# Kernel tuning notes

Hardware: AMD Instinct MI355X
Metric: run time of the kernel (lower is better)

The kernel has to match this reference:

```python
import jax, jax.numpy as jnp
import numpy as np

H, D = 16, 1024
HD = D // H  # 64

def setup_inputs() -> dict:
    key = jax.random.key(0)
    ks = jax.random.split(key, 11)
    B, S = 2, 2048
    s_in = 1.0 / np.sqrt(D)
    return {
        "V": jax.random.normal(ks[0], (B, S, D), jnp.float32),
        "K": jax.random.normal(ks[1], (B, S, D), jnp.float32),
        "Q": jax.random.normal(ks[2], (B, S, D), jnp.float32),
        # stacked per-head Linear weights, torch layout [out,in] -> [H, HD, D]
        "Wv": jax.random.normal(ks[3], (H, HD, D), jnp.float32) * s_in,
        "bv": jnp.zeros((H, HD), jnp.float32),
        "Wk": jax.random.normal(ks[4], (H, HD, D), jnp.float32) * s_in,
        "bk": jnp.zeros((H, HD), jnp.float32),
        "Wq": jax.random.normal(ks[5], (H, HD, D), jnp.float32) * s_in,
        "bq": jnp.zeros((H, HD), jnp.float32),
        "Wo": jax.random.normal(ks[6], (D, D), jnp.float32) * s_in,
        "bo": jnp.zeros((D,), jnp.float32),
    }

def reference(V, K, Q, Wv, bv, Wk, bk, Wq, bq, Wo, bo):
    scale = HD ** (-0.5)
    # per-head projections fused into one batched GEMM: [B,S,D] x [H,HD,D] -> [B,H,S,HD]
    q = jnp.einsum('bsd,hed->bhse', Q, Wq) + bq[None, :, None, :]
    k = jnp.einsum('bsd,hed->bhse', K, Wk) + bk[None, :, None, :]
    v = jnp.einsum('bsd,hed->bhse', V, Wv) + bv[None, :, None, :]
    # scaled dot-product attention
    scores = jnp.einsum('bhqe,bhke->bhqk', q, k) * scale  # [B,H,S,S]
    p = jax.nn.softmax(scores, axis=-1)
    att = jnp.einsum('bhqk,bhke->bhqe', p, v)  # [B,H,S,HD]
    # concat heads (head 0 first, matching the torch cat order) then output proj
    B, _, S, _ = att.shape
    cat = jnp.transpose(att, (0, 2, 1, 3)).reshape(B, S, H * HD)
    return cat @ Wo.T + bo
```

## Files before the change

### kernel.cpp

```cpp
#include <hip/hip_runtime.h>
#include <cstdint>
#include <cstddef>

typedef __bf16 bf16_t;
typedef bf16_t bf16x8 __attribute__((ext_vector_type(8)));
typedef bf16_t bf16x4 __attribute__((ext_vector_type(4)));
typedef float f32x4 __attribute__((ext_vector_type(4)));
typedef float f32x2 __attribute__((ext_vector_type(2)));

__device__ __forceinline__ void gl_lds16(const void* g, void* l) {
  __builtin_amdgcn_global_load_lds(
      (const __attribute__((address_space(1))) void*)g,
      (__attribute__((address_space(3))) void*)l, 16, 0, 0);
}

__device__ __forceinline__ f32x4 mfma16(bf16x8 a, bf16x8 b, f32x4 c) {
  return __builtin_amdgcn_mfma_f32_16x16x32_bf16(a, b, c, 0, 0, 0);
}

__device__ __forceinline__ float exp2_fast(float x) {
  float r;
  asm("v_exp_f32 %0, %1" : "=v"(r) : "v"(x));
  return r;
}

#define SCHED_FENCE() __builtin_amdgcn_sched_barrier(0)
#define WAIT_VM0()   do { asm volatile("s_waitcnt vmcnt(0)");   SCHED_FENCE(); } while (0)
#define WAIT_LGKM0() do { asm volatile("s_waitcnt lgkmcnt(0)"); SCHED_FENCE(); } while (0)
#define RAW_BAR()    do { __builtin_amdgcn_s_barrier();         SCHED_FENCE(); } while (0)

struct CvtArgs { const float* src[7]; bf16_t* dst[7]; };

__global__ __launch_bounds__(256) void convert_all(CvtArgs a) {
  unsigned g = blockIdx.x * 256u + threadIdx.x;
  unsigned seg, off;
  if (g < 524288u) {
    seg = g >> 17; off = g & 131071u;
  } else {
    unsigned h = g - 524288u;
    seg = 4u + (h >> 19); off = h & 524287u;
  }
  const float4* s = (const float4*)a.src[seg] + (size_t)off * 2;
  float4 x0 = s[0], x1 = s[1];
  bf16x8 o;
  o[0] = (bf16_t)x0.x; o[1] = (bf16_t)x0.y; o[2] = (bf16_t)x0.z; o[3] = (bf16_t)x0.w;
  o[4] = (bf16_t)x1.x; o[5] = (bf16_t)x1.y; o[6] = (bf16_t)x1.z; o[7] = (bf16_t)x1.w;
  *(bf16x8*)(a.dst[seg] + (size_t)off * 8) = o;
}

__device__ __forceinline__ void stage128(const bf16_t* src, bf16_t* dst, int t, int w) {
  #pragma unroll
  for (int i = 0; i < 4; i++) {
    int g = t + i * 256;
    int r = g >> 3, pc = g & 7;
    int lc = pc ^ (r & 7);
    gl_lds16(src + (size_t)r * 1024 + lc * 8, dst + i * 2048 + w * 512);
  }
}
__device__ __forceinline__ void stage64(const bf16_t* src, bf16_t* dst, int t, int w) {
  #pragma unroll
  for (int i = 0; i < 2; i++) {
    int g = t + i * 256;
    int r = g >> 3, pc = g & 7;
    int lc = pc ^ (r & 7);
    gl_lds16(src + (size_t)r * 1024 + lc * 8, dst + i * 2048 + w * 512);
  }
}

struct ProjArgs {
  const bf16_t* A[3]; const bf16_t* W[3]; const float* bias[3];
  bf16_t* out[3]; float scale[3];
};

__global__ __launch_bounds__(256, 2) void gemm_proj(ProjArgs p) {
  __shared__ __attribute__((aligned(16))) unsigned char smem[65536];
  const int z = blockIdx.z;
  const bf16_t* A = p.A[z] + (size_t)blockIdx.x * 128 * 1024;
  const bf16_t* W = p.W[z] + (size_t)blockIdx.y * 128 * 1024;

  const int t = threadIdx.x;
  const int w = t >> 6, l = t & 63;
  const int lq = l >> 4, lr = l & 15;
  const int mq = w & 1, nq = w >> 1;

  f32x4 acc[4][4];
  f32x4 zero = {0.f, 0.f, 0.f, 0.f};
  #pragma unroll
  for (int i = 0; i < 4; i++)
    #pragma unroll
    for (int j = 0; j < 4; j++) acc[i][j] = zero;

  stage128(A, (bf16_t*)smem, t, w);
  stage128(W, (bf16_t*)(smem + 16384), t, w);
  WAIT_VM0();
  RAW_BAR();

  for (int step = 0; step < 16; ++step) {
    const int cur = step & 1;
    bf16_t* as = (bf16_t*)(smem + cur * 32768);
    bf16_t* bs = (bf16_t*)(smem + cur * 32768 + 16384);
    if (step < 15) {
      bf16_t* an = (bf16_t*)(smem + (cur ^ 1) * 32768);
      stage128(A + (step + 1) * 64, an, t, w);
      stage128(W + (step + 1) * 64, an + 8192, t, w);
    }
    SCHED_FENCE();
    #pragma unroll
    for (int kk = 0; kk < 2; kk++) {
      bf16x8 af[4], bfr[4];
      #pragma unroll
      for (int i = 0; i < 4; i++) {
        int R = mq * 64 + i * 16 + lr;
        int ch = (kk * 4 + lq) ^ (R & 7);
        af[i] = *(const bf16x8*)(as + R * 64 + ch * 8);
      }
      #pragma unroll
      for (int j = 0; j < 4; j++) {
        int R = nq * 64 + j * 16 + lr;
        int ch = (kk * 4 + lq) ^ (R & 7);
        bfr[j] = *(const bf16x8*)(bs + R * 64 + ch * 8);
      }
      __builtin_amdgcn_s_setprio(1);
      #pragma unroll
      for (int i = 0; i < 4; i++)
        #pragma unroll
        for (int j = 0; j < 4; j++)
          acc[i][j] = mfma16(af[i], bfr[j], acc[i][j]);
      __builtin_amdgcn_s_setprio(0);
    }
    WAIT_VM0();
    RAW_BAR();
  }

  const float* bias = p.bias[z];
  const float scale = p.scale[z];
  __syncthreads();
  bf16_t* ts = (bf16_t*)smem;
  #pragma unroll
  for (int i = 0; i < 4; i++) {
    #pragma unroll
    for (int j = 0; j < 4; j++) {
      int nl = nq * 64 + j * 16 + lr;
      float bz = bias[blockIdx.y * 128 + nl];
      #pragma unroll
      for (int r = 0; r < 4; r++) {
        int ml = mq * 64 + i * 16 + lq * 4 + r;
        bf16_t val = (bf16_t)((acc[i][j][r] + bz) * scale);
        if (z == 0) {
          int mlp = (ml & 96) | (((ml >> 2) & 3) << 3) | (((ml >> 4) & 1) << 2) | (ml & 3);
          ts[nl * 136 + mlp] = val;
        } else {
          ts[ml * 136 + nl] = val;
        }
      }
    }
  }
  __syncthreads();
  bf16_t* out = p.out[z];
  const int b = blockIdx.x >> 4, sbase = (blockIdx.x & 15) * 128;
  if (z == 0) {
    #pragma unroll
    for (int ii = 0; ii < 8; ii++) {
      int idx = t * 8 + ii * 2048;
      int rr = idx >> 7, cc = idx & 127;
      int n = blockIdx.y * 128 + rr;
      int h = n >> 6, e = n & 63;
      bf16x8 vq = *(const bf16x8*)(ts + rr * 136 + cc);
      *(bf16x8*)(out + ((size_t)(b * 16 + h) * 64 + e) * 2048 + sbase + cc) = vq;
    }
  } else {
    #pragma unroll
    for (int ii = 0; ii < 8; ii++) {
      int idx = t * 8 + ii * 2048;
      int rr = idx >> 7, cc = idx & 127;
      int n = blockIdx.y * 128 + cc;
      int h = n >> 6, e = n & 63;
      bf16x8 vq = *(const bf16x8*)(ts + rr * 136 + cc);
      *(bf16x8*)(out + ((size_t)(b * 16 + h) * 2048 + sbase + rr) * 64 + e) = vq;
    }
  }
}

__global__ __launch_bounds__(256, 2) void attn(
    const bf16_t* __restrict__ qw, const bf16_t* __restrict__ kw,
    const bf16_t* __restrict__ vtw, bf16_t* __restrict__ att)
{
  __shared__ __attribute__((aligned(16))) unsigned char smem[32768];
  const int bh = blockIdx.x, qt = blockIdx.y;
  const int t = threadIdx.x, w = t >> 6, l = t & 63, lq = l >> 4, lr = l & 15;

  const bf16_t* kb0 = kw + (size_t)bh * 131072;
  const bf16_t* vb0 = vtw + (size_t)bh * 131072;
  bf16_t* qstage = (bf16_t*)(smem + 16384);

  const bf16_t* qbase = qw + ((size_t)bh * 2048 + qt * 128) * 64;
  #pragma unroll
  for (int i = 0; i < 4; i++) {
    int g = t + i * 256;
    int r = g >> 3, pc = g & 7;
    int lc = pc ^ (r & 7);
    gl_lds16(qbase + (size_t)r * 64 + lc * 8, qstage + i * 2048 + w * 512);
  }
  #pragma unroll
  for (int i = 0; i < 2; i++) {
    int g = t + i * 256;
    int r = g >> 3, pc = g & 7;
    int lc = pc ^ (r & 7);
    gl_lds16(kb0 + (size_t)r * 64 + lc * 8, (bf16_t*)smem + i * 2048 + w * 512);
    gl_lds16(vb0 + (size_t)r * 2048 + lc * 8, (bf16_t*)(smem + 8192) + i * 2048 + w * 512);
  }
  WAIT_VM0();
  RAW_BAR();
  bf16x8 qf[2][2];
  #pragma unroll
  for (int gq = 0; gq < 2; gq++)
    #pragma unroll
    for (int kk = 0; kk < 2; kk++) {
      int R = w * 32 + gq * 16 + lr;
      int ch = (kk * 4 + lq) ^ (R & 7);
      qf[gq][kk] = *(const bf16x8*)(qstage + R * 64 + ch * 8);
    }
  WAIT_LGKM0();
  RAW_BAR();

  f32x4 O[2][4];
  f32x4 zero = {0.f, 0.f, 0.f, 0.f};
  #pragma unroll
  for (int gq = 0; gq < 2; gq++)
    #pragma unroll
    for (int et = 0; et < 4; et++) O[gq][et] = zero;
  f32x2 lsv[2];
  lsv[0] = f32x2{0.f, 0.f}; lsv[1] = f32x2{0.f, 0.f};
  bf16x8 vf[8];
  bf16x8 pbA[2][2], pbB[2][2];

#define ATTN_BODY(KT, CUR, PBOUT, PBIN, FIRST, DOSTAGE)                          \
  {                                                                              \
    bf16_t* ksb = (bf16_t*)(smem + (CUR) * 16384);                               \
    bf16_t* vsb = (bf16_t*)(smem + (CUR) * 16384 + 8192);                        \
    if (DOSTAGE) {                                                               \
      bf16_t* kn = (bf16_t*)(smem + ((CUR) ^ 1) * 16384);                        \
      const bf16_t* kbase = kb0 + (size_t)((KT) + 1) * 4096;                     \
      const bf16_t* vbase = vb0 + (size_t)((KT) + 1) * 64;                       \
      _Pragma("unroll")                                                          \
      for (int i = 0; i < 2; i++) {                                              \
        int g = t + i * 256;                                                     \
        int r = g >> 3, pc = g & 7;                                              \
        int lc = pc ^ (r & 7);                                                   \
        gl_lds16(kbase + (size_t)r * 64 + lc * 8, kn + i * 2048 + w * 512);      \
        gl_lds16(vbase + (size_t)r * 2048 + lc * 8, kn + 4096 + i * 2048 + w * 512); \
      }                                                                          \
    }                                                                            \
    f32x4 sc[2][4];                                                              \
    _Pragma("unroll")                                                            \
    for (int gq = 0; gq < 2; gq++)                                               \
      _Pragma("unroll")                                                          \
      for (int j = 0; j < 4; j++) sc[gq][j] = zero;                              \
    __builtin_amdgcn_s_setprio(1);                                               \
    if (!(FIRST)) {                                                              \
      _Pragma("unroll")                                                          \
      for (int ks2 = 0; ks2 < 2; ks2++)                                          \
        _Pragma("unroll")                                                        \
        for (int et = 0; et < 4; et++) {                                         \
          O[0][et] = mfma16(vf[ks2 * 4 + et], (PBIN)[0][ks2], O[0][et]);         \
          O[1][et] = mfma16(vf[ks2 * 4 + et], (PBIN)[1][ks2], O[1][et]);         \
        }                                                                        \
    }                                                                            \
    _Pragma("unroll")                                                            \
    for (int kk = 0; kk < 2; kk++)                                               \
      _Pragma("unroll")                                                          \
      for (int j = 0; j < 4; j++) {                                              \
        int R = j * 16 + lr;                                                     \
        int ch = (kk * 4 + lq) ^ (R & 7);                                        \
        bf16x8 kf = *(const bf16x8*)(ksb + R * 64 + ch * 8);                     \
        sc[0][j] = mfma16(kf, qf[0][kk], sc[0][j]);                              \
        sc[1][j] = mfma16(kf, qf[1][kk], sc[1][j]);                              \
      }                                                                          \
    __builtin_amdgcn_s_setprio(0);                                               \
    _Pragma("unroll")                                                            \
    for (int ks2 = 0; ks2 < 2; ks2++)                                            \
      _Pragma("unroll")                                                          \
      for (int et = 0; et < 4; et++) {                                           \
        int R = et * 16 + lr;                                                    \
        int ch = (ks2 * 4 + lq) ^ (R & 7);                                       \
        vf[ks2 * 4 + et] = *(const bf16x8*)(vsb + R * 64 + ch * 8);              \
      }                                                                          \
    _Pragma("unroll")                                                            \
    for (int gq = 0; gq < 2; gq++)                                               \
      _Pragma("unroll")                                                          \
      for (int ks2 = 0; ks2 < 2; ks2++)                                          \
        _Pragma("unroll")                                                        \
        for (int r = 0; r < 4; r++) {                                            \
          float e0 = exp2_fast(sc[gq][2 * ks2][r]);                              \
          float e1 = exp2_fast(sc[gq][2 * ks2 + 1][r]);                          \
          f32x2 ee = {e0, e1};                                                   \
          lsv[gq] += ee;                                                         \
          (PBOUT)[gq][ks2][r] = (bf16_t)e0;                                      \
          (PBOUT)[gq][ks2][4 + r] = (bf16_t)e1;                                  \
        }                                                                        \
    WAIT_LGKM0();         \
    if (DOSTAGE) WAIT_VM0();                             \
    RAW_BAR();                                                                   \
  }

  ATTN_BODY(0, 0, pbA, pbB, true, true);
  ATTN_BODY(1, 1, pbB, pbA, false, true);
  for (int kt2 = 1; kt2 < 16; ++kt2) {
    const int kt = kt2 * 2;
    ATTN_BODY(kt, 0, pbA, pbB, false, true);
    ATTN_BODY(kt + 1, 1, pbB, pbA, false, (kt2 < 15));
  }
#undef ATTN_BODY

  #pragma unroll
  for (int ks2 = 0; ks2 < 2; ks2++)
    #pragma unroll
    for (int et = 0; et < 4; et++) {
      O[0][et] = mfma16(vf[ks2 * 4 + et], pbB[0][ks2], O[0][et]);
      O[1][et] = mfma16(vf[ks2 * 4 + et], pbB[1][ks2], O[1][et]);
    }

  float s0 = lsv[0][0] + lsv[0][1];
  float s1 = lsv[1][0] + lsv[1][1];
  s0 += __shfl_xor(s0, 16);
  s0 += __shfl_xor(s0, 32);
  s1 += __shfl_xor(s1, 16);
  s1 += __shfl_xor(s1, 32);
  float rinv[2] = {1.0f / s0, 1.0f / s1};

  bf16_t* ts = (bf16_t*)smem;
  #pragma unroll
  for (int gq = 0; gq < 2; gq++)
    #pragma unroll
    for (int et = 0; et < 4; et++) {
      bf16x4 pv;
      #pragma unroll
      for (int r = 0; r < 4; r++) pv[r] = (bf16_t)(O[gq][et][r] * rinv[gq]);
      *(bf16x4*)(ts + (w * 32 + gq * 16 + lr) * 72 + et * 16 + lq * 4) = pv;
    }
  __syncthreads();
  const int b = bh >> 4, h = bh & 15;
  #pragma unroll
  for (int i = 0; i < 4; i++) {
    int c = t + i * 256;
    int row = c >> 3, c8 = c & 7;
    bf16x8 vv = *(const bf16x8*)(ts + row * 72 + c8 * 8);
    *(bf16x8*)(att + ((size_t)b * 2048 + qt * 128 + row) * 1024 + h * 64 + c8 * 8) = vv;
  }
}

__global__ __launch_bounds__(256, 3) void gemm_out(
    const bf16_t* __restrict__ A, const bf16_t* __restrict__ W,
    const float* __restrict__ bias, float* __restrict__ out)
{
  __shared__ __attribute__((aligned(16))) unsigned char smem[49152];
  const bf16_t* Ab = A + (size_t)blockIdx.x * 64 * 1024;
  const bf16_t* Wb = W + (size_t)blockIdx.y * 128 * 1024;
  const int t = threadIdx.x, w = t >> 6, l = t & 63, lq = l >> 4, lr = l & 15;
  const int mh = w & 1, nh = w >> 1;

  f32x4 acc[2][4];
  f32x4 zero = {0.f, 0.f, 0.f, 0.f};
  #pragma unroll
  for (int i = 0; i < 2; i++)
    #pragma unroll
    for (int j = 0; j < 4; j++) acc[i][j] = zero;

  stage64(Ab, (bf16_t*)smem, t, w);
  stage128(Wb, (bf16_t*)(smem + 8192), t, w);
  WAIT_VM0();
  RAW_BAR();

  for (int step = 0; step < 16; ++step) {
    const int cur = step & 1;
    bf16_t* as = (bf16_t*)(smem + cur * 24576);
    bf16_t* bs = (bf16_t*)(smem + cur * 24576 + 8192);
    if (step < 15) {
      bf16_t* an = (bf16_t*)(smem + (cur ^ 1) * 24576);
      stage64(Ab + (step + 1) * 64, an, t, w);
      stage128(Wb + (step + 1) * 64, an + 4096, t, w);
    }
    SCHED_FENCE();
    #pragma unroll
    for (int kk = 0; kk < 2; kk++) {
      bf16x8 af[2], bfr[4];
      #pragma unroll
      for (int i = 0; i < 2; i++) {
        int R = mh * 32 + i * 16 + lr;
        int ch = (kk * 4 + lq) ^ (R & 7);
        af[i] = *(const bf16x8*)(as + R * 64 + ch * 8);
      }
      #pragma unroll
      for (int j = 0; j < 4; j++) {
        int R = nh * 64 + j * 16 + lr;
        int ch = (kk * 4 + lq) ^ (R & 7);
        bfr[j] = *(const bf16x8*)(bs + R * 64 + ch * 8);
      }
      __builtin_amdgcn_s_setprio(1);
      #pragma unroll
      for (int i = 0; i < 2; i++)
        #pragma unroll
        for (int j = 0; j < 4; j++)
          acc[i][j] = mfma16(af[i], bfr[j], acc[i][j]);
      __builtin_amdgcn_s_setprio(0);
    }
    WAIT_VM0();
    RAW_BAR();
  }

  #pragma unroll
  for (int i = 0; i < 2; i++) {
    #pragma unroll
    for (int j = 0; j < 4; j++) {
      int col = blockIdx.y * 128 + nh * 64 + j * 16 + lr;
      float bz = bias[col];
      #pragma unroll
      for (int r = 0; r < 4; r++) {
        int row = blockIdx.x * 64 + mh * 32 + i * 16 + lq * 4 + r;
        out[(size_t)row * 1024 + col] = acc[i][j][r] + bz;
      }
    }
  }
}

extern "C" void kernel_launch(void* const* d_in, const int* in_sizes, int n_in,
                              void* d_out, int out_size, void* d_ws, size_t ws_size,
                              hipStream_t stream) {
  (void)in_sizes; (void)n_in; (void)out_size;
  const float* V  = (const float*)d_in[0];
  const float* Kx = (const float*)d_in[1];
  const float* Q  = (const float*)d_in[2];
  const float* Wv = (const float*)d_in[3];
  const float* bv = (const float*)d_in[4];
  const float* Wk = (const float*)d_in[5];
  const float* bk = (const float*)d_in[6];
  const float* Wq = (const float*)d_in[7];
  const float* bq = (const float*)d_in[8];
  const float* Wo = (const float*)d_in[9];
  const float* bo = (const float*)d_in[10];

  const size_t E = 1048576;
  if (ws_size < 20 * E * sizeof(bf16_t)) return;

  bf16_t* ws = (bf16_t*)d_ws;
  bf16_t* cWo   = ws;
  bf16_t* cWv   = ws + E;
  bf16_t* cWk   = ws + 2 * E;
  bf16_t* cWq   = ws + 3 * E;
  bf16_t* q_ws  = ws + 4 * E;
  bf16_t* k_ws  = ws + 8 * E;
  bf16_t* vt_ws = ws + 12 * E;
  bf16_t* att_ws= ws + 16 * E;

  bf16_t* cV = att_ws;
  bf16_t* cK = (bf16_t*)d_out;
  bf16_t* cQ = (bf16_t*)d_out + 4 * E;

  CvtArgs ca;
  ca.src[0] = Wo; ca.src[1] = Wv; ca.src[2] = Wk; ca.src[3] = Wq;
  ca.src[4] = V;  ca.src[5] = Kx; ca.src[6] = Q;
  ca.dst[0] = cWo; ca.dst[1] = cWv; ca.dst[2] = cWk; ca.dst[3] = cWq;
  ca.dst[4] = cV;  ca.dst[5] = cK;  ca.dst[6] = cQ;
  convert_all<<<8192, 256, 0, stream>>>(ca);

  ProjArgs pa;
  pa.A[0] = cV;  pa.A[1] = cK;  pa.A[2] = cQ;
  pa.W[0] = cWv; pa.W[1] = cWk; pa.W[2] = cWq;
  pa.bias[0] = bv; pa.bias[1] = bk; pa.bias[2] = bq;
  pa.out[0] = vt_ws; pa.out[1] = k_ws; pa.out[2] = q_ws;
  pa.scale[0] = 1.f; pa.scale[1] = 1.f; pa.scale[2] = 0.125f * 1.4426950408889634f;
  gemm_proj<<<dim3(32, 8, 3), 256, 0, stream>>>(pa);

  attn<<<dim3(32, 16), 256, 0, stream>>>(q_ws, k_ws, vt_ws, att_ws);

  gemm_out<<<dim3(64, 8), 256, 0, stream>>>(att_ws, cWo, bo, (float*)d_out);
}
```

Measured before the change: 205.4 us.

## Triple-buffer K/V tiles in attention with prefetch distance two

```diff
diff --git a/kernel.cpp b/kernel.cpp
--- a/kernel.cpp
+++ b/kernel.cpp
@@ -185,13 +185,13 @@
     const bf16_t* __restrict__ qw, const bf16_t* __restrict__ kw,
     const bf16_t* __restrict__ vtw, bf16_t* __restrict__ att)
 {
-  __shared__ __attribute__((aligned(16))) unsigned char smem[32768];
+  __shared__ __attribute__((aligned(16))) unsigned char smem[49152];
   const int bh = blockIdx.x, qt = blockIdx.y;
   const int t = threadIdx.x, w = t >> 6, l = t & 63, lq = l >> 4, lr = l & 15;
 
   const bf16_t* kb0 = kw + (size_t)bh * 131072;
   const bf16_t* vb0 = vtw + (size_t)bh * 131072;
-  bf16_t* qstage = (bf16_t*)(smem + 16384);
+  bf16_t* qstage = (bf16_t*)(smem + 32768);
 
   const bf16_t* qbase = qw + ((size_t)bh * 2048 + qt * 128) * 64;
   #pragma unroll
@@ -202,14 +202,21 @@
     gl_lds16(qbase + (size_t)r * 64 + lc * 8, qstage + i * 2048 + w * 512);
   }
   #pragma unroll
-  for (int i = 0; i < 2; i++) {
-    int g = t + i * 256;
-    int r = g >> 3, pc = g & 7;
-    int lc = pc ^ (r & 7);
-    gl_lds16(kb0 + (size_t)r * 64 + lc * 8, (bf16_t*)smem + i * 2048 + w * 512);
-    gl_lds16(vb0 + (size_t)r * 2048 + lc * 8, (bf16_t*)(smem + 8192) + i * 2048 + w * 512);
-  }
-  WAIT_VM0();
+  for (int tt = 0; tt < 2; tt++) {
+    bf16_t* kn = (bf16_t*)(smem + tt * 16384);
+    const bf16_t* kbase = kb0 + (size_t)tt * 4096;
+    const bf16_t* vbase = vb0 + (size_t)tt * 64;
+    #pragma unroll
+    for (int i = 0; i < 2; i++) {
+      int g = t + i * 256;
+      int r = g >> 3, pc = g & 7;
+      int lc = pc ^ (r & 7);
+      gl_lds16(kbase + (size_t)r * 64 + lc * 8, kn + i * 2048 + w * 512);
+      gl_lds16(vbase + (size_t)r * 2048 + lc * 8, kn + 4096 + i * 2048 + w * 512);
+    }
+  }
+  asm volatile("s_waitcnt vmcnt(8)");
+  SCHED_FENCE();
   RAW_BAR();
   bf16x8 qf[2][2];
   #pragma unroll
@@ -220,7 +227,8 @@
       int ch = (kk * 4 + lq) ^ (R & 7);
       qf[gq][kk] = *(const bf16x8*)(qstage + R * 64 + ch * 8);
     }
-  WAIT_LGKM0();
+  asm volatile("s_waitcnt vmcnt(4) lgkmcnt(0)");
+  SCHED_FENCE();
   RAW_BAR();
 
   f32x4 O[2][4];
@@ -231,17 +239,17 @@
     for (int et = 0; et < 4; et++) O[gq][et] = zero;
   f32x2 lsv[2];
   lsv[0] = f32x2{0.f, 0.f}; lsv[1] = f32x2{0.f, 0.f};
-  bf16x8 vf[8];
+  bf16x8 vfA[8], vfB[8];
   bf16x8 pbA[2][2], pbB[2][2];
 
-#define ATTN_BODY(KT, CUR, PBOUT, PBIN, FIRST, DOSTAGE)                          \
+#define ATTN_BODY(KT, BUF, NBUF, PBOUT, PBIN, VFOUT, VFIN, FIRST, DOSTAGE, ENDWAIT) \
   {                                                                              \
-    bf16_t* ksb = (bf16_t*)(smem + (CUR) * 16384);                               \
-    bf16_t* vsb = (bf16_t*)(smem + (CUR) * 16384 + 8192);                        \
+    bf16_t* ksb = (bf16_t*)(smem + (BUF) * 16384);                               \
+    bf16_t* vsb = (bf16_t*)(smem + (BUF) * 16384 + 8192);                        \
     if (DOSTAGE) {                                                               \
-      bf16_t* kn = (bf16_t*)(smem + ((CUR) ^ 1) * 16384);                        \
-      const bf16_t* kbase = kb0 + (size_t)((KT) + 1) * 4096;                     \
-      const bf16_t* vbase = vb0 + (size_t)((KT) + 1) * 64;                       \
+      bf16_t* kn = (bf16_t*)(smem + (NBUF) * 16384);                             \
+      const bf16_t* kbase = kb0 + (size_t)((KT) + 2) * 4096;                     \
+      const bf16_t* vbase = vb0 + (size_t)((KT) + 2) * 64;                       \
       _Pragma("unroll")                                                          \
       for (int i = 0; i < 2; i++) {                                              \
         int g = t + i * 256;                                                     \
@@ -251,6 +259,7 @@
         gl_lds16(vbase + (size_t)r * 2048 + lc * 8, kn + 4096 + i * 2048 + w * 512); \
       }                                                                          \
     }                                                                            \
+    SCHED_FENCE();                                                               \
     f32x4 sc[2][4];                                                              \
     _Pragma("unroll")                                                            \
     for (int gq = 0; gq < 2; gq++)                                               \
@@ -262,8 +271,8 @@
       for (int ks2 = 0; ks2 < 2; ks2++)                                          \
         _Pragma("unroll")                                                        \
         for (int et = 0; et < 4; et++) {                                         \
-          O[0][et] = mfma16(vf[ks2 * 4 + et], (PBIN)[0][ks2], O[0][et]);         \
-          O[1][et] = mfma16(vf[ks2 * 4 + et], (PBIN)[1][ks2], O[1][et]);         \
+          O[0][et] = mfma16((VFIN)[ks2 * 4 + et], (PBIN)[0][ks2], O[0][et]);     \
+          O[1][et] = mfma16((VFIN)[ks2 * 4 + et], (PBIN)[1][ks2], O[1][et]);     \
         }                                                                        \
     }                                                                            \
     _Pragma("unroll")                                                            \
@@ -283,7 +292,7 @@
       for (int et = 0; et < 4; et++) {                                           \
         int R = et * 16 + lr;                                                    \
         int ch = (ks2 * 4 + lq) ^ (R & 7);                                       \
-        vf[ks2 * 4 + et] = *(const bf16x8*)(vsb + R * 64 + ch * 8);              \
+        (VFOUT)[ks2 * 4 + et] = *(const bf16x8*)(vsb + R * 64 + ch * 8);         \
       }                                                                          \
     _Pragma("unroll")                                                            \
     for (int gq = 0; gq < 2; gq++)                                               \
@@ -298,26 +307,37 @@
           (PBOUT)[gq][ks2][r] = (bf16_t)e0;                                      \
           (PBOUT)[gq][ks2][4 + r] = (bf16_t)e1;                                  \
         }                                                                        \
-    WAIT_LGKM0();         \
-    if (DOSTAGE) WAIT_VM0();                             \
+          \
+          \
+    asm volatile("s_waitcnt vmcnt(" ENDWAIT ") lgkmcnt(0)");                     \
+    SCHED_FENCE();                                                               \
     RAW_BAR();                                                                   \
   }
 
-  ATTN_BODY(0, 0, pbA, pbB, true, true);
-  ATTN_BODY(1, 1, pbB, pbA, false, true);
-  for (int kt2 = 1; kt2 < 16; ++kt2) {
-    const int kt = kt2 * 2;
-    ATTN_BODY(kt, 0, pbA, pbB, false, true);
-    ATTN_BODY(kt + 1, 1, pbB, pbA, false, (kt2 < 15));
-  }
+  ATTN_BODY(0, 0, 2, pbA, pbB, vfA, vfB, true,  true, "4");
+  ATTN_BODY(1, 1, 0, pbB, pbA, vfB, vfA, false, true, "4");
+  ATTN_BODY(2, 2, 1, pbA, pbB, vfA, vfB, false, true, "4");
+  ATTN_BODY(3, 0, 2, pbB, pbA, vfB, vfA, false, true, "4");
+  ATTN_BODY(4, 1, 0, pbA, pbB, vfA, vfB, false, true, "4");
+  ATTN_BODY(5, 2, 1, pbB, pbA, vfB, vfA, false, true, "4");
+  for (int g6 = 6; g6 < 30; g6 += 6) {
+    ATTN_BODY(g6 + 0, 0, 2, pbA, pbB, vfA, vfB, false, true, "4");
+    ATTN_BODY(g6 + 1, 1, 0, pbB, pbA, vfB, vfA, false, true, "4");
+    ATTN_BODY(g6 + 2, 2, 1, pbA, pbB, vfA, vfB, false, true, "4");
+    ATTN_BODY(g6 + 3, 0, 2, pbB, pbA, vfB, vfA, false, true, "4");
+    ATTN_BODY(g6 + 4, 1, 0, pbA, pbB, vfA, vfB, false, true, "4");
+    ATTN_BODY(g6 + 5, 2, 1, pbB, pbA, vfB, vfA, false, true, "4");
+  }
+  ATTN_BODY(30, 0, 2, pbA, pbB, vfA, vfB, false, false, "0");
+  ATTN_BODY(31, 1, 0, pbB, pbA, vfB, vfA, false, false, "0");
 #undef ATTN_BODY
 
   #pragma unroll
   for (int ks2 = 0; ks2 < 2; ks2++)
     #pragma unroll
     for (int et = 0; et < 4; et++) {
-      O[0][et] = mfma16(vf[ks2 * 4 + et], pbB[0][ks2], O[0][et]);
-      O[1][et] = mfma16(vf[ks2 * 4 + et], pbB[1][ks2], O[1][et]);
+      O[0][et] = mfma16(vfB[ks2 * 4 + et], pbB[0][ks2], O[0][et]);
+      O[1][et] = mfma16(vfB[ks2 * 4 + et], pbB[1][ks2], O[1][et]);
     }
 
   float s0 = lsv[0][0] + lsv[0][1];
```

After: 204.7 us. Within noise of the previous version (-0.3%).
